# Optimization experiments

Measured on AMD Instinct MI355X. Metric: run time of the kernel, lower is better.

The kernel has to match this reference:

```python
import jax, jax.numpy as jnp
import numpy as np

B, N, D, R = 32, 1024, 1152, 4


def setup_inputs() -> dict:
    key = jax.random.key(0)
    ks = jax.random.split(key, 9)
    s = 1.0 / np.sqrt(D)
    return {
        "x": jax.random.normal(ks[0], (B, N, D), dtype=jnp.float32),
        "Wq": jax.random.uniform(ks[1], (D, D), jnp.float32, -s, s),
        "bq": jax.random.uniform(ks[2], (D,), jnp.float32, -s, s),
        "Wk": jax.random.uniform(ks[3], (D, D), jnp.float32, -s, s),
        "bk": jax.random.uniform(ks[4], (D,), jnp.float32, -s, s),
        "Wv": jax.random.uniform(ks[5], (D, D), jnp.float32, -s, s),
        "bv": jax.random.uniform(ks[6], (D,), jnp.float32, -s, s),
        "Wo": jax.random.uniform(ks[7], (D, D), jnp.float32, -s, s),
        "bo": jax.random.uniform(ks[8], (D,), jnp.float32, -s, s),
        "r": R,
    }


def _merge(t, r):
    # VisionTokenMerger: non-overlapping window-mean over r consecutive tokens.
    b, n, d = t.shape
    merged = t.reshape(b, n // r, r, d).mean(axis=2)  # [B, N/r, D]
    return merged, r  # num_patches_per_token is the scalar window size


def reference(x, Wq, bq, Wk, bk, Wv, bv, Wo, bo, r):
    Q = x @ Wq.T + bq
    K = x @ Wk.T + bk
    V = x @ Wv.T + bv
    K_m, npt = _merge(K, r)            # [B, M, D], M = N/r
    V_m, _ = _merge(V, r)
    scale = 1.0 / jnp.sqrt(jnp.float32(Q.shape[-1]))
    scores = jnp.einsum('bnd,bmd->bnm', Q, K_m) * scale
    scores = scores + jnp.log(jnp.float32(npt))  # log-count additive bias
    w = jax.nn.softmax(scores, axis=-1)
    out = jnp.einsum('bnm,bmd->bnd', w, V_m)
    return out @ Wo.T + bo
```

## Files before the change

kernel.cpp:

```cpp
#include <hip/hip_runtime.h>
#include <hip/hip_bf16.h>


typedef __bf16 bf16;
typedef __attribute__((ext_vector_type(8))) __bf16 bf16x8;
typedef __attribute__((ext_vector_type(4))) __bf16 bf16x4;
typedef __attribute__((ext_vector_type(4))) float f32x4;

#define GAS __attribute__((address_space(1)))
#define LAS __attribute__((address_space(3)))

__device__ __forceinline__ void async_copy16(const void* g, void* s) {
    __builtin_amdgcn_global_load_lds((GAS unsigned int*)g, (LAS unsigned int*)s, 16, 0, 0);
}

template <typename OutT, bool HAS_BIAS>
__global__ __launch_bounds__(256) void gemm_bt(
    const bf16* __restrict__ A, const bf16* __restrict__ B,
    const float* __restrict__ bias, OutT* __restrict__ C,
    int N, int K, int lda, int ldb, int ldc, float scale,
    long sAb, long sBb, long sCb) {
    __shared__ __align__(16) bf16 As[2][128 * 32];
    __shared__ __align__(16) bf16 Bs[2][128 * 32];
    const int tid  = threadIdx.x;
    const int wave = tid >> 6;
    const int lane = tid & 63;
    const int quad = lane >> 4;
    const int l16  = lane & 15;
    const int wM   = (wave >> 1) * 64;
    const int wN   = (wave & 1) * 64;

    int bx = blockIdx.x, by = blockIdx.y;
    const int nbx = gridDim.x, nby = gridDim.y;
    if (((nby & 7) == 0) && (nbx % 9 == 0)) {
        int lid = by * nbx + bx;
        int xcd = lid & 7;
        int s   = lid >> 3;
        int Pn  = nby >> 3;
        int gsz = 9 * Pn;
        int g   = s / gsz;
        int rem = s - g * gsz;
        int p   = rem / 9;
        by = p * 8 + xcd;
        bx = g * 9 + (rem - p * 9);
    }

    const long zb = blockIdx.z;
    A += zb * sAb;
    B += zb * sBb;
    C += zb * sCb;

    const int rowBase = by * 128;
    const int colBase = bx * 128;

    const int g0 = wave * 64 + lane;
    const int r0 = g0 >> 2;
    const int c0 = (g0 & 3) * 8;
    const bf16* a0 = A + (long)(rowBase + r0) * lda + c0;
    const bf16* a1 = A + (long)(rowBase + 64 + r0) * lda + c0;
    const bf16* b0 = B + (long)(colBase + r0) * ldb + c0;
    const bf16* b1 = B + (long)(colBase + 64 + r0) * ldb + c0;
    char* lA = (char*)As + wave * 1024;
    char* lB = (char*)Bs + wave * 1024;

    f32x4 acc[4][4] = {};

    const int kt = K >> 5;
    async_copy16(a0, lA);
    async_copy16(a1, lA + 4096);
    async_copy16(b0, lB);
    async_copy16(b1, lB + 4096);
    a0 += 32; a1 += 32; b0 += 32; b1 += 32;
    int cur = 0;
    for (int k = 0; k < kt; ++k) {
        __syncthreads();
        if (k + 1 < kt) {
            char* nA = lA + ((cur ^ 1) << 13);
            char* nB = lB + ((cur ^ 1) << 13);
            async_copy16(a0, nA);
            async_copy16(a1, nA + 4096);
            async_copy16(b0, nB);
            async_copy16(b1, nB + 4096);
            a0 += 32; a1 += 32; b0 += 32; b1 += 32;
        }
        const bf16* Ab = &As[cur][0];
        const bf16* Bb = &Bs[cur][0];
        bf16x8 af[4], bfv[4];
#pragma unroll
        for (int t = 0; t < 4; ++t) {
            af[t]  = *(const bf16x8*)(Ab + (wM + t * 16 + l16) * 32 + quad * 8);
            bfv[t] = *(const bf16x8*)(Bb + (wN + t * 16 + l16) * 32 + quad * 8);
        }
#pragma unroll
        for (int mt = 0; mt < 4; ++mt)
#pragma unroll
            for (int nt = 0; nt < 4; ++nt)
                acc[mt][nt] = __builtin_amdgcn_mfma_f32_16x16x32_bf16(
                    af[mt], bfv[nt], acc[mt][nt], 0, 0, 0);
        cur ^= 1;
    }

#pragma unroll
    for (int mt = 0; mt < 4; ++mt) {
        const int row = rowBase + wM + mt * 16 + quad * 4;
#pragma unroll
        for (int nt = 0; nt < 4; ++nt) {
            const int col = colBase + wN + nt * 16 + l16;
            const float bv = HAS_BIAS ? bias[col] : 0.0f;
#pragma unroll
            for (int r = 0; r < 4; ++r) {
                float v = acc[mt][nt][r] * scale + bv;
                C[(long)(row + r) * ldc + col] = (OutT)v;
            }
        }
    }
}

__global__ __launch_bounds__(256) void scores_softmax_k(
    const bf16* __restrict__ X, const bf16* __restrict__ UVW,
    const float* __restrict__ cvec, bf16* __restrict__ P) {
    __shared__ __align__(16) bf16 As[2][64 * 32];
    __shared__ __align__(16) bf16 Bs[2][256 * 32];
    __shared__ float red[64][4];
    __shared__ float red2[64][4];
    const int tid  = threadIdx.x;
    const int wave = tid >> 6;
    const int lane = tid & 63;
    const int quad = lane >> 4;
    const int l16  = lane & 15;
    const int wN   = wave * 64;
    const int wc   = wave;

    int bx = blockIdx.x, by = blockIdx.y;
    {
        int lid = by * 16 + bx;
        int xcd = lid & 7;
        int s   = lid >> 3;
        by = (s >> 4) * 8 + xcd;
        bx = s & 15;
    }
    const long b = by;
    const bf16* A = X + (b * 1024 + (long)bx * 64) * 1152;
    const bf16* B = UVW + b * 256 * 2304;

    const int ra = tid >> 2, ca = (tid & 3) * 8;
    const bf16* a0 = A + (long)ra * 1152 + ca;
    const bf16* b0 = B + (long)ra * 2304 + ca;
    const bf16* b1 = B + (long)(64 + ra) * 2304 + ca;
    const bf16* b2 = B + (long)(128 + ra) * 2304 + ca;
    const bf16* b3 = B + (long)(192 + ra) * 2304 + ca;
    char* lA = (char*)As + wave * 1024;
    char* lB = (char*)Bs + wave * 1024;

    f32x4 acc[4][4] = {};
    async_copy16(a0, lA);
    async_copy16(b0, lB);
    async_copy16(b1, lB + 4096);
    async_copy16(b2, lB + 8192);
    async_copy16(b3, lB + 12288);
    a0 += 32; b0 += 32; b1 += 32; b2 += 32; b3 += 32;
    int cur = 0;
#pragma unroll 1
    for (int k = 0; k < 36; ++k) {
        __syncthreads();
        if (k < 35) {
            char* nA = lA + ((cur ^ 1) << 12);
            char* nB = lB + ((cur ^ 1) << 14);
            async_copy16(a0, nA);
            async_copy16(b0, nB);
            async_copy16(b1, nB + 4096);
            async_copy16(b2, nB + 8192);
            async_copy16(b3, nB + 12288);
            a0 += 32; b0 += 32; b1 += 32; b2 += 32; b3 += 32;
        }
        const bf16* Ab = &As[cur][0];
        const bf16* Bb = &Bs[cur][0];
        bf16x8 af[4], bfv[4];
#pragma unroll
        for (int t = 0; t < 4; ++t) {
            af[t]  = *(const bf16x8*)(Ab + (t * 16 + l16) * 32 + quad * 8);
            bfv[t] = *(const bf16x8*)(Bb + (wN + t * 16 + l16) * 32 + quad * 8);
        }
#pragma unroll
        for (int mt = 0; mt < 4; ++mt)
#pragma unroll
            for (int nt = 0; nt < 4; ++nt)
                acc[mt][nt] = __builtin_amdgcn_mfma_f32_16x16x32_bf16(
                    af[mt], bfv[nt], acc[mt][nt], 0, 0, 0);
        cur ^= 1;
    }

    float cv[4];
#pragma unroll
    for (int nt = 0; nt < 4; ++nt) cv[nt] = cvec[b * 256 + wN + nt * 16 + l16];
#pragma unroll
    for (int mt = 0; mt < 4; ++mt)
#pragma unroll
        for (int nt = 0; nt < 4; ++nt)
#pragma unroll
            for (int r = 0; r < 4; ++r) acc[mt][nt][r] += cv[nt];

    const float scale = 0.029462782549439484f;

#pragma unroll
    for (int mt = 0; mt < 4; ++mt)
#pragma unroll
        for (int r = 0; r < 4; ++r) {
            float pm = fmaxf(fmaxf(acc[mt][0][r], acc[mt][1][r]),
                             fmaxf(acc[mt][2][r], acc[mt][3][r]));
#pragma unroll
            for (int off = 1; off <= 8; off <<= 1) pm = fmaxf(pm, __shfl_xor(pm, off));
            if (l16 == 0) red[mt * 16 + quad * 4 + r][wc] = pm;
        }
    __syncthreads();
#pragma unroll
    for (int mt = 0; mt < 4; ++mt)
#pragma unroll
        for (int r = 0; r < 4; ++r) {
            const int R = mt * 16 + quad * 4 + r;
            float4 q = *(const float4*)red[R];
            float m = fmaxf(fmaxf(q.x, q.y), fmaxf(q.z, q.w));
            float ps = 0.0f;
#pragma unroll
            for (int nt = 0; nt < 4; ++nt) {
                float e = __expf((acc[mt][nt][r] - m) * scale);
                acc[mt][nt][r] = e;
                ps += e;
            }
#pragma unroll
            for (int off = 1; off <= 8; off <<= 1) ps += __shfl_xor(ps, off);
            if (l16 == 0) red2[R][wc] = ps;
        }
    __syncthreads();
#pragma unroll
    for (int mt = 0; mt < 4; ++mt)
#pragma unroll
        for (int r = 0; r < 4; ++r) {
            const int R = mt * 16 + quad * 4 + r;
            float4 q = *(const float4*)red2[R];
            float inv = 1.0f / (q.x + q.y + q.z + q.w);
            const long gr = b * 1024 + (long)bx * 64 + R;
#pragma unroll
            for (int nt = 0; nt < 4; ++nt)
                P[gr * 256 + wN + nt * 16 + l16] = (bf16)(acc[mt][nt][r] * inv);
        }
}

__global__ void cvt_wT_k(const float* __restrict__ Wq, const float* __restrict__ Wk,
                         const float* __restrict__ Wv, const float* __restrict__ Wo,
                         bf16* __restrict__ dst) {
    const int z = blockIdx.z;
    const int r0 = blockIdx.y * 64, c0 = blockIdx.x * 64;
    const int tid = threadIdx.x;
    if (z == 3) {
        int row = tid >> 2;
        int col = (tid & 3) * 16;
        const float* s = Wo + (long)(r0 + row) * 1152 + c0 + col;
        bf16* d = dst + 1327104 + (long)(r0 + row) * 1152 + c0 + col;
#pragma unroll
        for (int j = 0; j < 4; ++j) {
            float4 v = ((const float4*)s)[j];
            bf16x4 o = {(bf16)v.x, (bf16)v.y, (bf16)v.z, (bf16)v.w};
            ((bf16x4*)d)[j] = o;
        }
        return;
    }
    __shared__ bf16 t[64][66];
    const float* src = z == 0 ? Wq : z == 1 ? Wk : Wv;
    bf16* d = dst + (long)(z == 0 ? 0 : z == 1 ? 2 : 3) * 1327104;
    {
        int row = tid >> 4;
        int col4 = (tid & 15) * 4;
#pragma unroll
        for (int p = 0; p < 4; ++p) {
            int r = row + p * 16;
            float4 v = *(const float4*)(src + (long)(r0 + r) * 1152 + c0 + col4);
            t[col4 + 0][r] = (bf16)v.x;
            t[col4 + 1][r] = (bf16)v.y;
            t[col4 + 2][r] = (bf16)v.z;
            t[col4 + 3][r] = (bf16)v.w;
        }
    }
    __syncthreads();
    {
        int orow = tid >> 2;
        int oc = (tid & 3) * 16;
        bf16x8 a, b2;
#pragma unroll
        for (int j = 0; j < 8; ++j) { a[j] = t[orow][oc + j]; b2[j] = t[orow][oc + 8 + j]; }
        bf16* o = d + (long)(c0 + orow) * 1152 + r0 + oc;
        *(bf16x8*)o = a;
        *(bf16x8*)(o + 8) = b2;
    }
}

__global__ void cvt_merge_x_k(const float* __restrict__ x, bf16* __restrict__ xb,
                              bf16* __restrict__ xm) {
    int i = blockIdx.x * 256 + threadIdx.x;
    int w = i / 288;
    int c4 = i - w * 288;
    const float4* p = (const float4*)(x + (long)w * 4608) + c4;
    float4 a = p[0], b = p[288], c = p[576], d = p[864];
    bf16x4 oa = {(bf16)a.x, (bf16)a.y, (bf16)a.z, (bf16)a.w};
    bf16x4 ob = {(bf16)b.x, (bf16)b.y, (bf16)b.z, (bf16)b.w};
    bf16x4 oc = {(bf16)c.x, (bf16)c.y, (bf16)c.z, (bf16)c.w};
    bf16x4 od = {(bf16)d.x, (bf16)d.y, (bf16)d.z, (bf16)d.w};
    bf16* base = xb + (long)w * 4608 + c4 * 4;
    *(bf16x4*)(base)        = oa;
    *(bf16x4*)(base + 1152) = ob;
    *(bf16x4*)(base + 2304) = oc;
    *(bf16x4*)(base + 3456) = od;
    float4 s;
    s.x = (a.x + b.x + c.x + d.x) * 0.25f;
    s.y = (a.y + b.y + c.y + d.y) * 0.25f;
    s.z = (a.z + b.z + c.z + d.z) * 0.25f;
    s.w = (a.w + b.w + c.w + d.w) * 0.25f;
    bf16x4 o = {(bf16)s.x, (bf16)s.y, (bf16)s.z, (bf16)s.w};
    *(bf16x4*)(xm + (long)w * 1152 + c4 * 4) = o;
}

__global__ void rowdot2_k(const bf16* __restrict__ WkT, const bf16* __restrict__ Wo_b,
                          const float* __restrict__ bq, const float* __restrict__ bv,
                          float* __restrict__ vk, float* __restrict__ biasUV) {
    const int z = blockIdx.y;
    const bf16* M = z ? Wo_b : WkT;
    const float* v = z ? bv : bq;
    const int row = blockIdx.x * 4 + (threadIdx.x >> 6);
    const int lane = threadIdx.x & 63;
    const bf16* mr = M + (long)row * 1152;
    float acc = 0.0f;
#pragma unroll
    for (int j = 0; j < 18; ++j)
        acc += (float)mr[j * 64 + lane] * v[j * 64 + lane];
#pragma unroll
    for (int off = 32; off; off >>= 1) acc += __shfl_xor(acc, off, 64);
    if (lane == 0) {
        if (z) biasUV[1152 + row] = acc;
        else { vk[row] = acc; biasUV[row] = 0.0f; }
    }
}

__global__ void rowdot_k(const bf16* __restrict__ M, const float* __restrict__ v,
                         float* __restrict__ out) {
    const int row = blockIdx.x * 4 + (threadIdx.x >> 6);
    const int lane = threadIdx.x & 63;
    const bf16* mr = M + (long)row * 1152;
    float acc = 0.0f;
#pragma unroll
    for (int j = 0; j < 18; ++j)
        acc += (float)mr[j * 64 + lane] * v[j * 64 + lane];
#pragma unroll
    for (int off = 32; off; off >>= 1) acc += __shfl_xor(acc, off, 64);
    if (lane == 0) out[row] = acc;
}

__global__ void transpose_vm_k(const bf16* __restrict__ UVW, bf16* __restrict__ VT) {
    __shared__ bf16 t[64][65];
    const int tid = threadIdx.x;
    const int b = blockIdx.z;
    const int d0 = blockIdx.x * 64, m0 = blockIdx.y * 64;
#pragma unroll
    for (int p = 0; p < 2; ++p) {
        int r = (tid >> 3) + p * 32;
        int c = (tid & 7) * 8;
        bf16x8 v = *(const bf16x8*)(UVW + (long)(b * 256 + m0 + r) * 2304 + 1152 + d0 + c);
#pragma unroll
        for (int j = 0; j < 8; ++j) t[c + j][r] = v[j];
    }
    __syncthreads();
#pragma unroll
    for (int p = 0; p < 2; ++p) {
        int r = (tid >> 3) + p * 32;
        int c = (tid & 7) * 8;
        bf16x8 o;
#pragma unroll
        for (int j = 0; j < 8; ++j) o[j] = t[r][c + j];
        *(bf16x8*)(VT + (long)b * 294912 + (long)(d0 + r) * 256 + m0 + c) = o;
    }
}

extern "C" void kernel_launch(void* const* d_in, const int* in_sizes, int n_in,
                              void* d_out, int out_size, void* d_ws, size_t ws_size,
                              hipStream_t stream) {
    const float* x  = (const float*)d_in[0];
    const float* Wq = (const float*)d_in[1];
    const float* bq = (const float*)d_in[2];
    const float* Wk = (const float*)d_in[3];
    const float* bk = (const float*)d_in[4];  (void)bk;
    const float* Wv = (const float*)d_in[5];
    const float* bv = (const float*)d_in[6];
    const float* Wo = (const float*)d_in[7];
    const float* bo = (const float*)d_in[8];
    float* out = (float*)d_out;
    char* ws = (char*)d_ws;

    bf16* WT4    = (bf16*)(ws);
    bf16* WkT_b  = WT4 + 2 * 1327104;
    bf16* Wo_b   = WT4 + 1 * 1327104;
    bf16* WQK2   = (bf16*)(ws + 10616832);
    float* biasUV = (float*)(ws + 15925248);
    float* vk     = (float*)(ws + 15934464);
    float* cvec   = (float*)(ws + 15939072);
    bf16* xm_b   = (bf16*)(ws + 15971840);
    bf16* UVW    = (bf16*)(ws + 34846208);
    bf16* VWT    = (bf16*)(ws + 72594944);
    bf16* P_b    = (bf16*)(ws + 91469312);

    bf16* x_b = (bf16*)d_out;

    cvt_wT_k<<<dim3(18, 18, 4), 256, 0, stream>>>(Wq, Wk, Wv, Wo, WT4);
    cvt_merge_x_k<<<9216, 256, 0, stream>>>(x, x_b, xm_b);

    rowdot2_k<<<dim3(288, 2), 256, 0, stream>>>(WkT_b, Wo_b, bq, bv, vk, biasUV);

    rowdot_k<<<2048, 256, 0, stream>>>(xm_b, vk, cvec);

    gemm_bt<bf16, false><<<dim3(9, 9, 2), 256, 0, stream>>>(
        WT4, WT4 + 2 * 1327104, nullptr, WQK2,
        1152, 1152, 1152, 1152, 1152, 1.0f, 1327104, 1327104, 1327104);

    gemm_bt<bf16, true><<<dim3(18, 64, 1), 256, 0, stream>>>(
        xm_b, WQK2, biasUV, UVW, 2304, 1152, 1152, 1152, 2304, 1.0f, 0, 0, 0);

    transpose_vm_k<<<dim3(18, 4, 32), 256, 0, stream>>>(UVW, VWT);

    scores_softmax_k<<<dim3(16, 32), 256, 0, stream>>>(x_b, UVW, cvec, P_b);

    gemm_bt<float, true><<<dim3(9, 8, 32), 256, 0, stream>>>(
        P_b, VWT, bo, out, 1152, 256, 256, 256, 1152, 1.0f,
        1024L * 256, 1152L * 256, 1024L * 1152);
}
```

Measured before the change: 489.3 us.

## Fuse softmax and P·V output projection into one attention kernel

Merges the scores/softmax kernel with the following P×VWT GEMM. The normalized probabilities stay in shared memory, and VWT tiles are streamed through double-buffered LDS to produce the fp32 output with bias, so the bf16 P matrix is never written to or read back from global memory. The bf16 copy of x, which lives in the output buffer, is relaid so that each block's x rows sit in the second half of its own output region, avoiding overwriting data other blocks still need. In exchange each block loops over 9 column chunks serially with only 512 blocks, which limits parallelism and adds LDS pressure (about 52KB).

```diff
diff --git a/kernel.cpp b/kernel.cpp
--- a/kernel.cpp
+++ b/kernel.cpp
@@ -116,20 +116,19 @@
     }
 }
 
-__global__ __launch_bounds__(256) void scores_softmax_k(
-    const bf16* __restrict__ X, const bf16* __restrict__ UVW,
-    const float* __restrict__ cvec, bf16* __restrict__ P) {
-    __shared__ __align__(16) bf16 As[2][64 * 32];
-    __shared__ __align__(16) bf16 Bs[2][256 * 32];
-    __shared__ float red[64][4];
-    __shared__ float red2[64][4];
+__global__ __launch_bounds__(256) void attn_k(
+    const bf16* Xb, const bf16* __restrict__ UVW, const bf16* __restrict__ VWT,
+    const float* __restrict__ cvec, const float* __restrict__ bo, float* out) {
+    __shared__ __align__(16) char smem[53248];
+    float* red  = (float*)(smem + 51200);
+    float* red2 = (float*)(smem + 52224);
+
     const int tid  = threadIdx.x;
     const int wave = tid >> 6;
     const int lane = tid & 63;
     const int quad = lane >> 4;
     const int l16  = lane & 15;
     const int wN   = wave * 64;
-    const int wc   = wave;
 
     int bx = blockIdx.x, by = blockIdx.y;
     {
@@ -140,8 +139,10 @@
         bx = s & 15;
     }
     const long b = by;
-    const bf16* A = X + (b * 1024 + (long)bx * 64) * 1152;
+    const int blk = (int)b * 16 + bx;
+    const bf16* A = Xb + (long)blk * 147456 + 73728;
     const bf16* B = UVW + b * 256 * 2304;
+    const bf16* VWTb = VWT + b * 294912;
 
     const int ra = tid >> 2, ca = (tid & 3) * 8;
     const bf16* a0 = A + (long)ra * 1152 + ca;
@@ -149,8 +150,8 @@
     const bf16* b1 = B + (long)(64 + ra) * 2304 + ca;
     const bf16* b2 = B + (long)(128 + ra) * 2304 + ca;
     const bf16* b3 = B + (long)(192 + ra) * 2304 + ca;
-    char* lA = (char*)As + wave * 1024;
-    char* lB = (char*)Bs + wave * 1024;
+    char* lA = smem + wave * 1024;
+    char* lB = smem + 8192 + wave * 1024;
 
     f32x4 acc[4][4] = {};
     async_copy16(a0, lA);
@@ -173,8 +174,8 @@
             async_copy16(b3, nB + 12288);
             a0 += 32; b0 += 32; b1 += 32; b2 += 32; b3 += 32;
         }
-        const bf16* Ab = &As[cur][0];
-        const bf16* Bb = &Bs[cur][0];
+        const bf16* Ab = (const bf16*)(smem + cur * 4096);
+        const bf16* Bb = (const bf16*)(smem + 8192 + cur * 16384);
         bf16x8 af[4], bfv[4];
 #pragma unroll
         for (int t = 0; t < 4; ++t) {
@@ -202,6 +203,14 @@
 
     const float scale = 0.029462782549439484f;
 
+    auto stageB = [&](int ch, int kk, int buf) {
+        const bf16* src = VWTb + (long)(ch * 128 + wave * 32 + (lane >> 2)) * 256
+                        + kk * 32 + (lane & 3) * 8;
+        char* dst = smem + 34816 + buf * 8192 + wave * 2048;
+        async_copy16(src, dst);
+        async_copy16(src + 16 * 256, dst + 1024);
+    };
+
 #pragma unroll
     for (int mt = 0; mt < 4; ++mt)
 #pragma unroll
@@ -210,15 +219,16 @@
                              fmaxf(acc[mt][2][r], acc[mt][3][r]));
 #pragma unroll
             for (int off = 1; off <= 8; off <<= 1) pm = fmaxf(pm, __shfl_xor(pm, off));
-            if (l16 == 0) red[mt * 16 + quad * 4 + r][wc] = pm;
+            if (l16 == 0) red[(mt * 16 + quad * 4 + r) * 4 + wave] = pm;
         }
     __syncthreads();
+    stageB(0, 0, 0);
 #pragma unroll
     for (int mt = 0; mt < 4; ++mt)
 #pragma unroll
         for (int r = 0; r < 4; ++r) {
             const int R = mt * 16 + quad * 4 + r;
-            float4 q = *(const float4*)red[R];
+            float4 q = *(const float4*)(red + R * 4);
             float m = fmaxf(fmaxf(q.x, q.y), fmaxf(q.z, q.w));
             float ps = 0.0f;
 #pragma unroll
@@ -229,7 +239,7 @@
             }
 #pragma unroll
             for (int off = 1; off <= 8; off <<= 1) ps += __shfl_xor(ps, off);
-            if (l16 == 0) red2[R][wc] = ps;
+            if (l16 == 0) red2[R * 4 + wave] = ps;
         }
     __syncthreads();
 #pragma unroll
@@ -237,13 +247,47 @@
 #pragma unroll
         for (int r = 0; r < 4; ++r) {
             const int R = mt * 16 + quad * 4 + r;
-            float4 q = *(const float4*)red2[R];
+            float4 q = *(const float4*)(red2 + R * 4);
             float inv = 1.0f / (q.x + q.y + q.z + q.w);
-            const long gr = b * 1024 + (long)bx * 64 + R;
-#pragma unroll
-            for (int nt = 0; nt < 4; ++nt)
-                P[gr * 256 + wN + nt * 16 + l16] = (bf16)(acc[mt][nt][r] * inv);
-        }
+#pragma unroll
+            for (int nt = 0; nt < 4; ++nt) {
+                const int col = wN + nt * 16 + l16;
+                *(bf16*)(smem + R * 544 + col * 2) = (bf16)(acc[mt][nt][r] * inv);
+            }
+        }
+
+    const char* pA = smem + (wave * 16 + l16) * 544;
+#pragma unroll 1
+    for (int ch = 0; ch < 9; ++ch) {
+        f32x4 acc2[8];
+#pragma unroll
+        for (int nt = 0; nt < 8; ++nt) acc2[nt] = (f32x4){0.f, 0.f, 0.f, 0.f};
+#pragma unroll
+        for (int kk = 0; kk < 8; ++kk) {
+            __syncthreads();
+            {
+                int nx = ch * 8 + kk + 1;
+                if (nx < 72) stageB(nx >> 3, nx & 7, nx & 1);
+            }
+            const char* pb = smem + 34816 + (kk & 1) * 8192;
+            bf16x8 af = *(const bf16x8*)(pA + kk * 64 + quad * 16);
+#pragma unroll
+            for (int nt = 0; nt < 8; ++nt) {
+                bf16x8 bv8 = *(const bf16x8*)(pb + (nt * 16 + l16) * 64 + quad * 16);
+                acc2[nt] = __builtin_amdgcn_mfma_f32_16x16x32_bf16(af, bv8, acc2[nt], 0, 0, 0);
+            }
+        }
+        const int d0 = ch * 128;
+        const long orow = b * 1024 + (long)bx * 64 + wave * 16 + quad * 4;
+#pragma unroll
+        for (int nt = 0; nt < 8; ++nt) {
+            const int col = d0 + nt * 16 + l16;
+            const float bvv = bo[col];
+#pragma unroll
+            for (int r = 0; r < 4; ++r)
+                out[(orow + r) * 1152 + col] = acc2[nt][r] + bvv;
+        }
+    }
 }
 
 __global__ void cvt_wT_k(const float* __restrict__ Wq, const float* __restrict__ Wk,
@@ -305,7 +349,8 @@
     bf16x4 ob = {(bf16)b.x, (bf16)b.y, (bf16)b.z, (bf16)b.w};
     bf16x4 oc = {(bf16)c.x, (bf16)c.y, (bf16)c.z, (bf16)c.w};
     bf16x4 od = {(bf16)d.x, (bf16)d.y, (bf16)d.z, (bf16)d.w};
-    bf16* base = xb + (long)w * 4608 + c4 * 4;
+    bf16* base = xb + (long)(w >> 4) * 147456 + 73728
+               + (long)((w & 15) * 4) * 1152 + c4 * 4;
     *(bf16x4*)(base)        = oa;
     *(bf16x4*)(base + 1152) = ob;
     *(bf16x4*)(base + 2304) = oc;
@@ -404,7 +449,6 @@
     bf16* xm_b   = (bf16*)(ws + 15971840);
     bf16* UVW    = (bf16*)(ws + 34846208);
     bf16* VWT    = (bf16*)(ws + 72594944);
-    bf16* P_b    = (bf16*)(ws + 91469312);
 
     bf16* x_b = (bf16*)d_out;
 
@@ -424,9 +468,5 @@
 
     transpose_vm_k<<<dim3(18, 4, 32), 256, 0, stream>>>(UVW, VWT);
 
-    scores_softmax_k<<<dim3(16, 32), 256, 0, stream>>>(x_b, UVW, cvec, P_b);
-
-    gemm_bt<float, true><<<dim3(9, 8, 32), 256, 0, stream>>>(
-        P_b, VWT, bo, out, 1152, 256, 256, 256, 1152, 1.0f,
-        1024L * 256, 1152L * 256, 1024L * 1152);
-}
+    attn_k<<<dim3(16, 32), 256, 0, stream>>>(x_b, UVW, VWT, cvec, bo, out);
+}
```

New measurement: 465.9 us. -4.8%, faster.
